# Kernel tuning notes

Measured on AMD Instinct MI355X. Metric: run time of the kernel, lower is better.

Reference implementation:

```python
import jax, jax.numpy as jnp
import numpy as np

B, N = 512, 500  # batch (cells), n_nodes (genes)


def setup_inputs() -> dict:
    key = jax.random.key(0)
    k1, k2, k3, k4 = jax.random.split(key, 4)
    x = jax.random.normal(k1, (B, N), dtype=jnp.float32)
    # GumbelAdjacency edge logits (bicycle initializes these near a constant; random here)
    log_alpha = jax.random.normal(k2, (N, N), dtype=jnp.float32)
    # single Linear(n_nodes, n_nodes, bias=False) weight, torch layout [out, in]
    W = jax.random.normal(k3, (N, N), dtype=jnp.float32) / np.sqrt(N).astype(np.float32)
    # uniform noise consumed by the gumbel-sigmoid sampler (one draw per batch element)
    u = jax.random.uniform(k4, (B, N, N), dtype=jnp.float32)
    return {"x": x, "log_alpha": log_alpha, "W": W, "u": u}


def reference(x, log_alpha, W, u):
    # --- GumbelAdjacency.forward(num_batch): hard gumbel-sigmoid sample, tau=1 ---
    eps = 1e-6
    uc = jnp.clip(u, eps, 1.0 - eps)
    logistic = jnp.log(uc) - jnp.log(1.0 - uc)            # logistic(0,1) noise
    y_soft = jax.nn.sigmoid(log_alpha[None, :, :] + logistic)  # [B, N, N]
    y_hard = (y_soft > 0.5).astype(y_soft.dtype)
    adj = y_soft + jax.lax.stop_gradient(y_hard - y_soft)  # straight-through

    # --- per-node masked MLP loop, fused ---
    # original: f_x[b, i] = tanh( (mask_i * adj[b, :, i] * x[b]) @ W.T )[i]
    #                     = tanh( sum_{j != i} W[i, j] * adj[b, j, i] * x[b, j] )
    mask = 1.0 - jnp.eye(N, dtype=x.dtype)                # mask[j, i] = 0 iff j == i
    gated = adj * mask[None, :, :]                        # [B, j, i]
    f_x = jnp.tanh(jnp.einsum('bji,bj,ij->bi', gated, x, W))  # [B, N]
    return f_x
```

## Files before the change

kernel.cpp:

```cpp
#include <hip/hip_runtime.h>
#include <math.h>

#define NN 500
#define BB 512

__device__ __forceinline__ bool np_decision(float laf, float v) {
    float l1 = (float)log((double)v);
    float s  = 1.0f - v;
    float l2 = (float)log((double)s);
    float logistic = l1 - l2;
    float z  = laf + logistic;
    float e  = (float)exp(-(double)z);
    float d  = 1.0f + e;
    float y  = 1.0f / d;
    return y > 0.5f;
}

__global__ void prep_kernel(const float* __restrict__ la,
                            const float* __restrict__ W,
                            float* __restrict__ Ustar,
                            float* __restrict__ Wt) {
    int idx = blockIdx.x * blockDim.x + threadIdx.x;
    if (idx >= NN * NN) return;
    int j = idx / NN;
    int i = idx - j * NN;
    float laf = la[idx];

    const float LO = 1e-6f;
    const float HI = (float)(1.0 - 1e-6);

    float U;
    if (!np_decision(laf, HI)) {
        U = __builtin_inff();
    } else if (np_decision(laf, LO)) {
        U = 0.0f;
    } else {
        unsigned lo = __float_as_uint(LO);
        unsigned hi = __float_as_uint(HI);
        double T  = 1.0 / (1.0 + exp((double)laf));
        float  Tf = fminf(fmaxf((float)T, LO), HI);
        unsigned g = __float_as_uint(Tf);
        unsigned a = (g > lo + 1024u) ? g - 1024u : lo;
        unsigned b = (g + 1024u < hi) ? g + 1024u : hi;
        if (!np_decision(laf, __uint_as_float(b))) {
            lo = b;
        } else {
            hi = b;
            if (np_decision(laf, __uint_as_float(a))) hi = a; else lo = a;
        }
        while (hi - lo > 1u) {
            unsigned mid = lo + (hi - lo) / 2u;
            if (np_decision(laf, __uint_as_float(mid))) hi = mid; else lo = mid;
        }
        U = __uint_as_float(hi);
    }
    Ustar[idx] = U;
    Wt[idx] = (i == j) ? 0.0f : W[i * NN + j];
}

__global__ __launch_bounds__(256) void fused_kernel(
        const float* __restrict__ x,
        const float* __restrict__ u,
        const float* __restrict__ Ustar,
        const float* __restrict__ Wt,
        float* __restrict__ out) {
    __shared__ float xs[NN];
    const int b = blockIdx.x;
    const int t = threadIdx.x;
    for (int k = t; k < NN; k += 256) xs[k] = x[b * NN + k];
    __syncthreads();
    if (t >= NN / 2) return;

    const float2* __restrict__ u2 = (const float2*)(u + (size_t)b * NN * NN);
    const float2* __restrict__ w2 = (const float2*)Wt;
    const float2* __restrict__ t2 = (const float2*)Ustar;

    const float LO = 1e-6f;
    const float HI = (float)(1.0 - 1e-6);

    float acc0 = 0.0f, acc1 = 0.0f;
#pragma unroll 8
    for (int j = 0; j < NN; ++j) {
        const int k = j * (NN / 2) + t;
        float2 uv = u2[k];
        float2 wv = w2[k];
        float2 tv = t2[k];
        float  xj = xs[j];
        float uc0 = fminf(fmaxf(uv.x, LO), HI);
        float uc1 = fminf(fmaxf(uv.y, LO), HI);
        if (uc0 >= tv.x) acc0 += wv.x * xj;
        if (uc1 >= tv.y) acc1 += wv.y * xj;
    }
    float2 o;
    o.x = tanhf(acc0);
    o.y = tanhf(acc1);
    ((float2*)out)[b * (NN / 2) + t] = o;
}

extern "C" void kernel_launch(void* const* d_in, const int* in_sizes, int n_in,
                              void* d_out, int out_size, void* d_ws, size_t ws_size,
                              hipStream_t stream) {
    const float* x  = (const float*)d_in[0];
    const float* la = (const float*)d_in[1];
    const float* W  = (const float*)d_in[2];
    const float* u  = (const float*)d_in[3];
    float* out = (float*)d_out;

    float* Ustar = (float*)d_ws;
    float* Wt    = (float*)((char*)d_ws + (size_t)NN * NN * sizeof(float));

    int prep_blocks = (NN * NN + 255) / 256;
    prep_kernel<<<prep_blocks, 256, 0, stream>>>(la, W, Ustar, Wt);
    fused_kernel<<<BB, 256, 0, stream>>>(x, u, Ustar, Wt, out);
}
```

Before: 714.6 us.

## Split j-reduction across four blocks per batch and interleave W with thresholds

The main kernel now splits the j dimension into four chunks, launching four times as many blocks. Each block writes partial sums to a workspace, and a new reduce kernel sums them and applies tanh. The weight and threshold tables are also interleaved into one float2 array, so each thread does a single float4 load per row instead of two float2 loads. The aim is more parallelism and latency hiding for the memory-bound 512 MB stream of u, at the cost of an extra launch and partial-sum traffic.

After: 705.4 us. Within noise of the previous version (-1.3%).

```diff
diff --git a/kernel.cpp b/kernel.cpp
--- a/kernel.cpp
+++ b/kernel.cpp
@@ -3,6 +3,8 @@
 
 #define NN 500
 #define BB 512
+#define NCHUNK 4
+#define JCH (NN / NCHUNK)
 
 __device__ __forceinline__ bool np_decision(float laf, float v) {
     float l1 = (float)log((double)v);
@@ -18,8 +20,7 @@
 
 __global__ void prep_kernel(const float* __restrict__ la,
                             const float* __restrict__ W,
-                            float* __restrict__ Ustar,
-                            float* __restrict__ Wt) {
+                            float2* __restrict__ WU) {
     int idx = blockIdx.x * blockDim.x + threadIdx.x;
     if (idx >= NN * NN) return;
     int j = idx / NN;
@@ -54,47 +55,54 @@
         }
         U = __uint_as_float(hi);
     }
-    Ustar[idx] = U;
-    Wt[idx] = (i == j) ? 0.0f : W[i * NN + j];
+    float w = (i == j) ? 0.0f : W[i * NN + j];
+    WU[idx] = make_float2(w, U);
 }
 
 __global__ __launch_bounds__(256) void fused_kernel(
         const float* __restrict__ x,
         const float* __restrict__ u,
-        const float* __restrict__ Ustar,
-        const float* __restrict__ Wt,
-        float* __restrict__ out) {
-    __shared__ float xs[NN];
-    const int b = blockIdx.x;
+        const float4* __restrict__ WU4,
+        float* __restrict__ P) {
+    __shared__ float xs[JCH];
+    const int bid = blockIdx.x;
+    const int b = bid >> 2;
+    const int c = bid & 3;
+    const int j0 = c * JCH;
     const int t = threadIdx.x;
-    for (int k = t; k < NN; k += 256) xs[k] = x[b * NN + k];
+    if (t < JCH) xs[t] = x[b * NN + j0 + t];
     __syncthreads();
     if (t >= NN / 2) return;
 
-    const float2* __restrict__ u2 = (const float2*)(u + (size_t)b * NN * NN);
-    const float2* __restrict__ w2 = (const float2*)Wt;
-    const float2* __restrict__ t2 = (const float2*)Ustar;
+    const float2* __restrict__ u2 = (const float2*)(u + (size_t)b * NN * NN) + j0 * (NN / 2);
+    const float4* __restrict__ wu = WU4 + j0 * (NN / 2);
 
     const float LO = 1e-6f;
     const float HI = (float)(1.0 - 1e-6);
 
     float acc0 = 0.0f, acc1 = 0.0f;
-#pragma unroll 8
-    for (int j = 0; j < NN; ++j) {
+#pragma unroll 5
+    for (int j = 0; j < JCH; ++j) {
         const int k = j * (NN / 2) + t;
         float2 uv = u2[k];
-        float2 wv = w2[k];
-        float2 tv = t2[k];
+        float4 wv = wu[k];
         float  xj = xs[j];
         float uc0 = fminf(fmaxf(uv.x, LO), HI);
         float uc1 = fminf(fmaxf(uv.y, LO), HI);
-        if (uc0 >= tv.x) acc0 += wv.x * xj;
-        if (uc1 >= tv.y) acc1 += wv.y * xj;
+        if (uc0 >= wv.y) acc0 += wv.x * xj;
+        if (uc1 >= wv.w) acc1 += wv.z * xj;
     }
-    float2 o;
-    o.x = tanhf(acc0);
-    o.y = tanhf(acc1);
-    ((float2*)out)[b * (NN / 2) + t] = o;
+    float2 o = make_float2(acc0, acc1);
+    ((float2*)(P + (size_t)c * BB * NN + b * NN))[t] = o;
+}
+
+__global__ __launch_bounds__(256) void reduce_kernel(const float* __restrict__ P,
+                                                     float* __restrict__ out) {
+    int n = blockIdx.x * blockDim.x + threadIdx.x;
+    if (n >= BB * NN) return;
+    const int S = BB * NN;
+    float s = P[n] + P[S + n] + P[2 * S + n] + P[3 * S + n];
+    out[n] = tanhf(s);
 }
 
 extern "C" void kernel_launch(void* const* d_in, const int* in_sizes, int n_in,
@@ -106,10 +114,11 @@
     const float* u  = (const float*)d_in[3];
     float* out = (float*)d_out;
 
-    float* Ustar = (float*)d_ws;
-    float* Wt    = (float*)((char*)d_ws + (size_t)NN * NN * sizeof(float));
+    float2* WU = (float2*)d_ws;
+    float*  P  = (float*)((char*)d_ws + (size_t)NN * NN * sizeof(float2));
 
     int prep_blocks = (NN * NN + 255) / 256;
-    prep_kernel<<<prep_blocks, 256, 0, stream>>>(la, W, Ustar, Wt);
-    fused_kernel<<<BB, 256, 0, stream>>>(x, u, Ustar, Wt, out);
+    prep_kernel<<<prep_blocks, 256, 0, stream>>>(la, W, WU);
+    fused_kernel<<<BB * NCHUNK, 256, 0, stream>>>(x, u, (const float4*)WU, P);
+    reduce_kernel<<<(BB * NN + 255) / 256, 256, 0, stream>>>(P, out);
 }
```
